# Kernel optimization log

Hardware: AMD Instinct MI355X
Metric: run time of the kernel (lower is better)

The kernel has to match this reference:

```python
import jax, jax.numpy as jnp
import numpy as np


def _conv1x1(x, W, b):
    # 1x1 conv == per-pixel channel matmul: x [B,C,H,W], W [O,C], b [O]
    return jnp.einsum('bchw,oc->bohw', x, W) + b[None, :, None, None]


def setup_inputs() -> dict:
    key = jax.random.key(0)
    ks = jax.random.split(key, 9)
    B, C, H, W = 16, 512, 32, 32
    s = 1.0 / np.sqrt(C)
    inp = {
        'x': jax.random.normal(ks[0], (B, C, H, W), dtype=jnp.float32),
        'Wq': jax.random.normal(ks[1], (C, C), dtype=jnp.float32) * s,
        'bq': jax.random.normal(ks[2], (C,), dtype=jnp.float32) * 0.01,
        'Wk': jax.random.normal(ks[3], (C, C), dtype=jnp.float32) * s,
        'bk': jax.random.normal(ks[4], (C,), dtype=jnp.float32) * 0.01,
        'Wv': jax.random.normal(ks[5], (C, C), dtype=jnp.float32) * s,
        'bv': jax.random.normal(ks[6], (C,), dtype=jnp.float32) * 0.01,
        'Wo': jax.random.normal(ks[7], (C, C), dtype=jnp.float32) * s,
        'bo': jax.random.normal(ks[8], (C,), dtype=jnp.float32) * 0.01,
    }
    return inp


def reference(x, Wq, bq, Wk, bk, Wv, bv, Wo, bo):
    B, C, H, W = x.shape
    q = _conv1x1(x, Wq, bq)
    k = _conv1x1(x, Wk, bk)
    v = _conv1x1(x, Wv, bv)
    hw = H * W
    qf = q.reshape(B, C, hw)  # [B,C,HW]
    kf = k.reshape(B, C, hw)
    vf = v.reshape(B, C, hw)
    # scores[b,i,j] = sum_c q[b,c,i] * k[b,c,j], scaled by c^-0.5
    scores = jnp.einsum('bci,bcj->bij', qf, kf) * (C ** -0.5)
    attn = jax.nn.softmax(scores, axis=2)  # softmax over keys j
    # out[b,c,i] = sum_j v[b,c,j] * attn[b,i,j]
    out = jnp.einsum('bcj,bij->bci', vf, attn).reshape(B, C, H, W)
    out = _conv1x1(out, Wo, bo)
    return x + out
```

## Files before the change

kernel.cpp:

```cpp
#include <hip/hip_runtime.h>
#include <hip/hip_bf16.h>
#include <math.h>


typedef __bf16 bf16x8 __attribute__((ext_vector_type(8)));
typedef float  f32x4  __attribute__((ext_vector_type(4)));

__device__ __forceinline__ unsigned short f2bf(float f) {
    unsigned u = __float_as_uint(f);
    u += 0x7fff + ((u >> 16) & 1);
    return (unsigned short)(u >> 16);
}

__device__ __forceinline__ void gload_lds16(const void* g, void* l) {
    __builtin_amdgcn_global_load_lds(
        (const __attribute__((address_space(1))) void*)g,
        (__attribute__((address_space(3))) void*)l, 16, 0, 0);
}

struct GemmP {
    const unsigned short* A;
    const unsigned short* B;
    void* C;
    const float* bias;
    const float* resid;
    int M, N, K, ldA, ldB;
    long sA, sB, sC, sR;
    int ln_nn, ln_pb;
    float scale;
};

template<bool OUT_F32, int BIAS_MODE, bool RESID, int EXPM>
__device__ __forceinline__ void gemm_body(const GemmP p, int L,
                                          unsigned short* Als,
                                          unsigned short* Bls)
{
    const int xcd = L & 7;
    const int idx = L >> 3;
    const int bz  = xcd * 2 + (idx >> p.ln_pb);
    const int w   = idx & ((1 << p.ln_pb) - 1);
    const int m0  = (w >> p.ln_nn) << 7;
    const int n0  = (w & ((1 << p.ln_nn) - 1)) << 7;

    const unsigned short* A = p.A + bz * p.sA;
    const unsigned short* B = p.B + bz * p.sB;

    const int tid  = threadIdx.x;
    const int lane = tid & 63;
    const int wave = tid >> 6;
    const int wm   = wave >> 1;
    const int wn   = wave & 1;

    const int ar = lane >> 2;
    const int ak = ((lane & 3) ^ ((ar >> 1) & 3)) * 8;

    const unsigned short* agp = A + (long)(m0 + wave * 16 + ar) * p.ldA + ak;
    const unsigned short* bgp = B + (long)(n0 + wave * 16 + ar) * p.ldB + ak;
    const long aj = 64L * p.ldA;
    const long bj = 64L * p.ldB;

    const int fr = lane & 15;
    const int fq = lane >> 4;
    const int kphys = (fq ^ ((fr >> 1) & 3)) * 8;

    f32x4 acc[4][4] = {};
    f32x4 acc1[4] = {};
    bf16x8 ones;
    if constexpr (EXPM == 2) {
        #pragma unroll
        for (int i = 0; i < 8; ++i) ones[i] = (__bf16)1.0f;
    }

    const int nsteps = p.K >> 5;

    auto STAGE = [&](int sel) {
        unsigned short* a0 = Als + sel * 4096;
        unsigned short* b0 = Bls + sel * 4096;
        gload_lds16(agp,      a0 + wave * 512);
        gload_lds16(agp + aj, a0 + (wave + 4) * 512);
        gload_lds16(bgp,      b0 + wave * 512);
        gload_lds16(bgp + bj, b0 + (wave + 4) * 512);
        agp += 32; bgp += 32;
    };

    auto COMPUTE = [&](int sel) {
        const unsigned short* Ap = Als + sel * 4096;
        const unsigned short* Bp = Bls + sel * 4096;
        bf16x8 af[4], bfr[4];
        #pragma unroll
        for (int mt = 0; mt < 4; ++mt)
            af[mt] = *(const bf16x8*)&Ap[(wm * 64 + mt * 16 + fr) * 32 + kphys];
        #pragma unroll
        for (int nt = 0; nt < 4; ++nt)
            bfr[nt] = *(const bf16x8*)&Bp[(wn * 64 + nt * 16 + fr) * 32 + kphys];
        if constexpr (EXPM == 2) {
            #pragma unroll
            for (int mt = 0; mt < 4; ++mt)
                acc1[mt] = __builtin_amdgcn_mfma_f32_16x16x32_bf16(
                    af[mt], ones, acc1[mt], 0, 0, 0);
        }
        #pragma unroll
        for (int mt = 0; mt < 4; ++mt)
            #pragma unroll
            for (int nt = 0; nt < 4; ++nt)
                acc[mt][nt] = __builtin_amdgcn_mfma_f32_16x16x32_bf16(
                    af[mt], bfr[nt], acc[mt][nt], 0, 0, 0);
    };

    STAGE(0);
    STAGE(1);

    int bc = 0, bn = 1, bs = 2;
    for (int t = 0; t < nsteps - 1; ++t) {
        __builtin_amdgcn_sched_barrier(0);
        asm volatile("s_waitcnt vmcnt(4)" ::: "memory");
        __builtin_amdgcn_s_barrier();
        asm volatile("" ::: "memory");
        __builtin_amdgcn_sched_barrier(0);
        if (t + 2 < nsteps) STAGE(bs);
        COMPUTE(bc);
        const int tmp = bc; bc = bn; bn = bs; bs = tmp;
    }
    __builtin_amdgcn_sched_barrier(0);
    asm volatile("s_waitcnt vmcnt(0)" ::: "memory");
    __builtin_amdgcn_s_barrier();
    asm volatile("" ::: "memory");
    __builtin_amdgcn_sched_barrier(0);
    COMPUTE(bc);

    float* Cf = (float*)p.C + bz * p.sC;
    unsigned short* Ch = (unsigned short*)p.C + bz * p.sC;
    const float* resid = RESID ? (p.resid + bz * p.sR) : nullptr;
    const int N = p.N;

    if constexpr (EXPM == 1) {
        #pragma unroll
        for (int mt = 0; mt < 4; ++mt)
            #pragma unroll
            for (int r = 0; r < 4; ++r) {
                const int row = m0 + wm * 64 + mt * 16 + fq * 4 + r;
                #pragma unroll
                for (int nt = 0; nt < 4; ++nt) {
                    const int col = n0 + wn * 64 + nt * 16 + fr;
                    Ch[(long)row * N + col] = f2bf(__expf(acc[mt][nt][r] * p.scale));
                }
            }
    } else {
        #pragma unroll
        for (int mt = 0; mt < 4; ++mt) {
            float linv[4];
            if constexpr (EXPM == 2) {
                #pragma unroll
                for (int r = 0; r < 4; ++r)
                    linv[r] = 1.0f / acc1[mt][r];
            }
            #pragma unroll
            for (int nt = 0; nt < 4; ++nt) {
                const int col = n0 + wn * 64 + nt * 16 + fr;
                const float bn2 = (BIAS_MODE == 2) ? p.bias[col] : 0.0f;
                #pragma unroll
                for (int r = 0; r < 4; ++r) {
                    const int row = m0 + wm * 64 + mt * 16 + fq * 4 + r;
                    float val = acc[mt][nt][r] + bn2;
                    if (BIAS_MODE == 1) val += p.bias[row];
                    if constexpr (EXPM == 2) val *= linv[r];
                    const long o = (long)row * N + col;
                    if (RESID) val += resid[o];
                    if (OUT_F32) Cf[o] = val;
                    else         Ch[o] = f2bf(val);
                }
            }
        }
    }
}

template<bool OUT_F32, int BIAS_MODE, bool RESID, int EXPM>
__global__ __launch_bounds__(256, 3) void gemm_bt_mfma(GemmP p)
{
    __shared__ unsigned short Als[3 * 4096];
    __shared__ unsigned short Bls[3 * 4096];
    gemm_body<OUT_F32, BIAS_MODE, RESID, EXPM>(p, blockIdx.x, Als, Bls);
}

__global__ __launch_bounds__(256, 3) void gemm_qkv_fused(GemmP pqk, GemmP pv, int split)
{
    __shared__ unsigned short Als[3 * 4096];
    __shared__ unsigned short Bls[3 * 4096];
    if ((int)blockIdx.x < split)
        gemm_body<false, 2, false, 0>(pqk, blockIdx.x, Als, Bls);
    else
        gemm_body<false, 1, false, 0>(pv, blockIdx.x - split, Als, Bls);
}

__global__ __launch_bounds__(256) void prep_all(
    const float* __restrict__ x, unsigned short* __restrict__ xT,
    const float* __restrict__ Wq, const float* __restrict__ Wk,
    const float* __restrict__ Wv, const float* __restrict__ Wo,
    const float* __restrict__ bq, const float* __restrict__ bk,
    unsigned short* __restrict__ Wb, float* __restrict__ biasqk)
{
    const int b = blockIdx.x;
    const int t = threadIdx.x;
    if (b < 2048) {
        __shared__ unsigned short tlb[64 * 64];
        const int batch = b >> 7;
        const int rem = b & 127;
        const int c0 = (rem >> 4) * 64;
        const int p0 = (rem & 15) * 64;
        const float* xb = x + (long)batch * 524288;
        unsigned short* xTb = xT + (long)batch * 524288;
        const int lx = t & 15;
        const int ly = t >> 4;
        #pragma unroll
        for (int i = 0; i < 4; ++i) {
            const int c = ly + 16 * i;
            const float4 f = *(const float4*)&xb[(long)(c0 + c) * 1024 + p0 + lx * 4];
            ushort4 h;
            h.x = f2bf(f.x); h.y = f2bf(f.y); h.z = f2bf(f.z); h.w = f2bf(f.w);
            const int colp = (lx * 4) ^ (((c >> 3) & 7) << 3);
            *(ushort4*)&tlb[c * 64 + colp] = h;
        }
        __syncthreads();
        const int sx = t & 7;
        const int sy = t >> 3;
        #pragma unroll
        for (int i = 0; i < 2; ++i) {
            const int r = sy + 32 * i;
            ushort4 lo, hi;
            lo.x = tlb[(sx * 8 + 0) * 64 + (r ^ (sx << 3))];
            lo.y = tlb[(sx * 8 + 1) * 64 + (r ^ (sx << 3))];
            lo.z = tlb[(sx * 8 + 2) * 64 + (r ^ (sx << 3))];
            lo.w = tlb[(sx * 8 + 3) * 64 + (r ^ (sx << 3))];
            hi.x = tlb[(sx * 8 + 4) * 64 + (r ^ (sx << 3))];
            hi.y = tlb[(sx * 8 + 5) * 64 + (r ^ (sx << 3))];
            hi.z = tlb[(sx * 8 + 6) * 64 + (r ^ (sx << 3))];
            hi.w = tlb[(sx * 8 + 7) * 64 + (r ^ (sx << 3))];
            unsigned short* o = &xTb[(long)(p0 + r) * 512 + c0 + sx * 8];
            *(ushort4*)o = lo;
            *(ushort4*)(o + 4) = hi;
        }
    } else if (b < 3072) {
        const int wb = b - 2048;
        const float* srcs[4] = {Wq, Wk, Wv, Wo};
        const float* s = srcs[wb >> 8];
        unsigned short* d = Wb + (long)(wb >> 8) * 262144;
        const int i = ((wb & 255) * 256 + t) * 4;
        const float4 f = *(const float4*)(s + i);
        ushort4 h;
        h.x = f2bf(f.x); h.y = f2bf(f.y); h.z = f2bf(f.z); h.w = f2bf(f.w);
        *(ushort4*)(d + i) = h;
    } else {
        biasqk[t]       = bq[t];
        biasqk[256 + t] = bq[256 + t];
        biasqk[512 + t] = bk[t];
        biasqk[768 + t] = bk[256 + t];
    }
}

extern "C" void kernel_launch(void* const* d_in, const int* in_sizes, int n_in,
                              void* d_out, int out_size, void* d_ws, size_t ws_size,
                              hipStream_t stream)
{
    const float* x  = (const float*)d_in[0];
    const float* Wq = (const float*)d_in[1];
    const float* bq = (const float*)d_in[2];
    const float* Wk = (const float*)d_in[3];
    const float* bk = (const float*)d_in[4];
    const float* Wv = (const float*)d_in[5];
    const float* bv = (const float*)d_in[6];
    const float* Wo = (const float*)d_in[7];
    const float* bo = (const float*)d_in[8];
    float* out = (float*)d_out;

    const int Bn = 16, C = 512, HW = 1024;
    const long CHW = (long)C * HW;
    const long SHW = (long)HW * HW;

    unsigned short* xT   = (unsigned short*)d_ws;
    unsigned short* qkT  = xT + Bn * CHW;
    unsigned short* vB   = qkT + Bn * SHW;
    unsigned short* expS = vB + Bn * CHW;
    unsigned short* Wb   = expS + Bn * SHW;
    float* biasqk = (float*)(Wb + 4 * 262144);
    unsigned short* OT = xT;

    unsigned short* Wvb = Wb + 2 * 262144;
    unsigned short* Wob = Wb + 3 * 262144;

    const dim3 blk(256);
    const float scale = 0.044194173824159216f;

    prep_all<<<dim3(3073), blk, 0, stream>>>(x, xT, Wq, Wk, Wv, Wo, bq, bk,
                                             Wb, biasqk);

    GemmP pqk = { xT, Wb, qkT, biasqk, nullptr,
                  HW, 2 * C, C, C, C, CHW, 0, SHW, 0, 3, 6, 0.0f };
    GemmP pv  = { Wvb, xT, vB, bv, nullptr,
                  C, HW, C, C, C, 0, CHW, CHW, 0, 3, 5, 0.0f };
    gemm_qkv_fused<<<dim3(1536), blk, 0, stream>>>(pqk, pv, 1024);

    GemmP ps  = { qkT, qkT + C, expS, nullptr, nullptr,
                  HW, HW, C, 2 * C, 2 * C, SHW, SHW, SHW, 0, 3, 6, scale };
    gemm_bt_mfma<false, 0, false, 1><<<dim3(1024), blk, 0, stream>>>(ps);

    GemmP po  = { expS, vB, OT, nullptr, nullptr,
                  HW, C, HW, HW, HW, SHW, CHW, CHW, 0, 2, 5, 0.0f };
    gemm_bt_mfma<false, 0, false, 2><<<dim3(512), blk, 0, stream>>>(po);

    GemmP pout = { Wob, OT, out, bo, x,
                   C, HW, C, C, C, 0, CHW, CHW, CHW, 3, 5, 0.0f };
    gemm_bt_mfma<true, 1, true, 0><<<dim3(512), blk, 0, stream>>>(pout);
}
```

Before: 216.6 us.

## Fuse attention-V GEMM with output projection and residual in one kernel

Replaces the separate attn@V GEMM and the Wo projection GEMM with a single kernel. Each 512-thread block computes a 64-pixel by 512-channel tile of the normalized attention output, keeps it in LDS as bf16, then multiplies it by Wo and adds bias and residual. This removes the OT round-trip through global memory and one launch. In exchange there are only 256 blocks, larger LDS use, and Wo is reloaded from global by every block. Block-to-batch mapping is arranged by XCD index, and MFMA priority is raised during compute.

```diff
diff --git a/kernel.cpp b/kernel.cpp
--- a/kernel.cpp
+++ b/kernel.cpp
@@ -64,12 +64,6 @@
     const int kphys = (fq ^ ((fr >> 1) & 3)) * 8;
 
     f32x4 acc[4][4] = {};
-    f32x4 acc1[4] = {};
-    bf16x8 ones;
-    if constexpr (EXPM == 2) {
-        #pragma unroll
-        for (int i = 0; i < 8; ++i) ones[i] = (__bf16)1.0f;
-    }
 
     const int nsteps = p.K >> 5;
 
@@ -93,12 +87,6 @@
         #pragma unroll
         for (int nt = 0; nt < 4; ++nt)
             bfr[nt] = *(const bf16x8*)&Bp[(wn * 64 + nt * 16 + fr) * 32 + kphys];
-        if constexpr (EXPM == 2) {
-            #pragma unroll
-            for (int mt = 0; mt < 4; ++mt)
-                acc1[mt] = __builtin_amdgcn_mfma_f32_16x16x32_bf16(
-                    af[mt], ones, acc1[mt], 0, 0, 0);
-        }
         #pragma unroll
         for (int mt = 0; mt < 4; ++mt)
             #pragma unroll
@@ -148,12 +136,6 @@
     } else {
         #pragma unroll
         for (int mt = 0; mt < 4; ++mt) {
-            float linv[4];
-            if constexpr (EXPM == 2) {
-                #pragma unroll
-                for (int r = 0; r < 4; ++r)
-                    linv[r] = 1.0f / acc1[mt][r];
-            }
             #pragma unroll
             for (int nt = 0; nt < 4; ++nt) {
                 const int col = n0 + wn * 64 + nt * 16 + fr;
@@ -163,7 +145,6 @@
                     const int row = m0 + wm * 64 + mt * 16 + fq * 4 + r;
                     float val = acc[mt][nt][r] + bn2;
                     if (BIAS_MODE == 1) val += p.bias[row];
-                    if constexpr (EXPM == 2) val *= linv[r];
                     const long o = (long)row * N + col;
                     if (RESID) val += resid[o];
                     if (OUT_F32) Cf[o] = val;
@@ -190,6 +171,158 @@
         gemm_body<false, 2, false, 0>(pqk, blockIdx.x, Als, Bls);
     else
         gemm_body<false, 1, false, 0>(pv, blockIdx.x - split, Als, Bls);
+}
+
+__global__ __launch_bounds__(512, 2) void gemm_o_out(
+    const unsigned short* __restrict__ expS,
+    const unsigned short* __restrict__ vB,
+    const unsigned short* __restrict__ Wob,
+    const float* __restrict__ bo,
+    const float* __restrict__ x,
+    float* __restrict__ out)
+{
+    __shared__ unsigned short LDS[3 * 18432];
+
+    const int L   = blockIdx.x;
+    const int xcd = L & 7;
+    const int idx = L >> 3;
+    const int bz  = xcd * 2 + (idx >> 4);
+    const int p0  = (idx & 15) * 64;
+
+    const unsigned short* Ab = expS + (long)bz * 1048576;
+    const unsigned short* Bb = vB   + (long)bz * 524288;
+
+    const int tid  = threadIdx.x;
+    const int lane = tid & 63;
+    const int wave = tid >> 6;
+    const int wm   = wave >> 2;
+    const int wn   = wave & 3;
+
+    const int ar = lane >> 2;
+    const int ak = ((lane & 3) ^ ((ar >> 1) & 3)) * 8;
+
+    const unsigned short* agp = Ab + (long)(p0 + wave * 16 + ar) * 1024 + ak;
+    const unsigned short* bgp = Bb + (long)(wave * 64 + ar) * 1024 + ak;
+    const long bj = 16L * 1024;
+
+    const int fr = lane & 15;
+    const int fq = lane >> 4;
+    const int kph = (fq ^ ((fr >> 1) & 3)) * 8;
+
+    f32x4 acc[2][8] = {};
+    f32x4 acc1[2] = {};
+    bf16x8 ones;
+    #pragma unroll
+    for (int i = 0; i < 8; ++i) ones[i] = (__bf16)1.0f;
+
+    auto STAGE = [&](int sel) {
+        unsigned short* s0 = LDS + sel * 18432;
+        if (wave < 4) gload_lds16(agp, s0 + wave * 512);
+        unsigned short* b0 = s0 + 2048;
+        gload_lds16(bgp,          b0 + (wave * 4 + 0) * 512);
+        gload_lds16(bgp + bj,     b0 + (wave * 4 + 1) * 512);
+        gload_lds16(bgp + 2 * bj, b0 + (wave * 4 + 2) * 512);
+        gload_lds16(bgp + 3 * bj, b0 + (wave * 4 + 3) * 512);
+        agp += 32; bgp += 32;
+    };
+
+    auto COMPUTE = [&](int sel) {
+        const unsigned short* Ap = LDS + sel * 18432;
+        const unsigned short* Bp = Ap + 2048;
+        bf16x8 af[2], bfr[8];
+        #pragma unroll
+        for (int mt = 0; mt < 2; ++mt)
+            af[mt] = *(const bf16x8*)&Ap[(wm * 32 + mt * 16 + fr) * 32 + kph];
+        #pragma unroll
+        for (int nt = 0; nt < 8; ++nt)
+            bfr[nt] = *(const bf16x8*)&Bp[(wn * 128 + nt * 16 + fr) * 32 + kph];
+        __builtin_amdgcn_s_setprio(1);
+        #pragma unroll
+        for (int mt = 0; mt < 2; ++mt)
+            acc1[mt] = __builtin_amdgcn_mfma_f32_16x16x32_bf16(
+                af[mt], ones, acc1[mt], 0, 0, 0);
+        #pragma unroll
+        for (int mt = 0; mt < 2; ++mt)
+            #pragma unroll
+            for (int nt = 0; nt < 8; ++nt)
+                acc[mt][nt] = __builtin_amdgcn_mfma_f32_16x16x32_bf16(
+                    af[mt], bfr[nt], acc[mt][nt], 0, 0, 0);
+        __builtin_amdgcn_s_setprio(0);
+    };
+
+    STAGE(0); STAGE(1);
+
+    for (int t = 0; t < 31; ++t) {
+        __builtin_amdgcn_sched_barrier(0);
+        if (wave < 4) asm volatile("s_waitcnt vmcnt(5)" ::: "memory");
+        else          asm volatile("s_waitcnt vmcnt(4)" ::: "memory");
+        __builtin_amdgcn_s_barrier();
+        asm volatile("" ::: "memory");
+        __builtin_amdgcn_sched_barrier(0);
+        if (t + 2 < 32) STAGE((t + 2) % 3);
+        COMPUTE(t % 3);
+    }
+    __builtin_amdgcn_sched_barrier(0);
+    asm volatile("s_waitcnt vmcnt(0)" ::: "memory");
+    __builtin_amdgcn_s_barrier();
+    asm volatile("" ::: "memory");
+    __builtin_amdgcn_sched_barrier(0);
+    COMPUTE(31 % 3);
+
+    __syncthreads();
+    unsigned short* OTl = LDS;
+    #pragma unroll
+    for (int mt = 0; mt < 2; ++mt) {
+        float linv[4];
+        #pragma unroll
+        for (int r = 0; r < 4; ++r) linv[r] = 1.0f / acc1[mt][r];
+        #pragma unroll
+        for (int nt = 0; nt < 8; ++nt) {
+            const int c = wn * 128 + nt * 16 + fr;
+            #pragma unroll
+            for (int r = 0; r < 4; ++r) {
+                const int pl = wm * 32 + mt * 16 + fq * 4 + r;
+                OTl[pl * 520 + c] = f2bf(acc[mt][nt][r] * linv[r]);
+            }
+        }
+    }
+    __syncthreads();
+
+    const int mw = wave >> 1;
+    const int pw = wave & 1;
+    f32x4 acc2[8][2] = {};
+    for (int ks = 0; ks < 16; ++ks) {
+        bf16x8 af2[8], bf2[2];
+        #pragma unroll
+        for (int mt = 0; mt < 8; ++mt)
+            af2[mt] = *(const bf16x8*)&Wob[(long)(mw * 128 + mt * 16 + fr) * 512
+                                           + ks * 32 + fq * 8];
+        #pragma unroll
+        for (int nt = 0; nt < 2; ++nt)
+            bf2[nt] = *(const bf16x8*)&OTl[(pw * 32 + nt * 16 + fr) * 520
+                                           + ks * 32 + fq * 8];
+        #pragma unroll
+        for (int mt = 0; mt < 8; ++mt)
+            #pragma unroll
+            for (int nt = 0; nt < 2; ++nt)
+                acc2[mt][nt] = __builtin_amdgcn_mfma_f32_16x16x32_bf16(
+                    af2[mt], bf2[nt], acc2[mt][nt], 0, 0, 0);
+    }
+    float* Co = out + (long)bz * 524288;
+    const float* xr = x + (long)bz * 524288;
+    #pragma unroll
+    for (int mt = 0; mt < 8; ++mt) {
+        #pragma unroll
+        for (int nt = 0; nt < 2; ++nt) {
+            const int col = p0 + pw * 32 + nt * 16 + fr;
+            #pragma unroll
+            for (int r = 0; r < 4; ++r) {
+                const int row = mw * 128 + mt * 16 + fq * 4 + r;
+                const long o = (long)row * 1024 + col;
+                Co[o] = acc2[mt][nt][r] + bo[row] + xr[o];
+            }
+        }
+    }
 }
 
 __global__ __launch_bounds__(256) void prep_all(
@@ -272,7 +405,8 @@
     const float* bo = (const float*)d_in[8];
     float* out = (float*)d_out;
 
-    const int Bn = 16, C = 512, HW = 1024;
+    const int C = 512, HW = 1024;
+    const int Bn = 16;
     const long CHW = (long)C * HW;
     const long SHW = (long)HW * HW;
 
@@ -282,7 +416,6 @@
     unsigned short* expS = vB + Bn * CHW;
     unsigned short* Wb   = expS + Bn * SHW;
     float* biasqk = (float*)(Wb + 4 * 262144);
-    unsigned short* OT = xT;
 
     unsigned short* Wvb = Wb + 2 * 262144;
     unsigned short* Wob = Wb + 3 * 262144;
@@ -303,11 +436,5 @@
                   HW, HW, C, 2 * C, 2 * C, SHW, SHW, SHW, 0, 3, 6, scale };
     gemm_bt_mfma<false, 0, false, 1><<<dim3(1024), blk, 0, stream>>>(ps);
 
-    GemmP po  = { expS, vB, OT, nullptr, nullptr,
-                  HW, C, HW, HW, HW, SHW, CHW, CHW, 0, 2, 5, 0.0f };
-    gemm_bt_mfma<false, 0, false, 2><<<dim3(512), blk, 0, stream>>>(po);
-
-    GemmP pout = { Wob, OT, out, bo, x,
-                   C, HW, C, C, C, 0, CHW, CHW, CHW, 3, 5, 0.0f };
-    gemm_bt_mfma<true, 1, true, 0><<<dim3(512), blk, 0, stream>>>(pout);
-}
+    gemm_o_out<<<dim3(256), dim3(512), 0, stream>>>(expS, vB, Wob, bo, x, out);
+}
```

Measured after the change: 218.2 us. No clear change (+0.7%).
